# Optimization experiments

Measured on AMD Instinct MI355X. Metric: run time of the kernel, lower is better.

## Reference

```python
import jax, jax.numpy as jnp
import numpy as np

B, D, O, E, K, H = 8192, 1024, 1024, 8, 2, 512
LOAD_BALANCE_ALPHA = 0.01


def setup_inputs() -> dict:
    key = jax.random.key(0)
    ks = jax.random.split(key, 7)
    s = 0.02
    return {
        "x": jax.random.normal(ks[0], (B, D), dtype=jnp.float32),
        "gate_W": jax.random.normal(ks[1], (D, E), dtype=jnp.float32) * s,
        "gate_b": jnp.zeros((E,), dtype=jnp.float32),
        "W1": jax.random.normal(ks[2], (E, D, H), dtype=jnp.float32) * s,
        "b1": jnp.zeros((E, H), dtype=jnp.float32),
        "W2": jax.random.normal(ks[3], (E, H, O), dtype=jnp.float32) * s,
        "b2": jnp.zeros((E, O), dtype=jnp.float32),
    }


def reference(x, gate_W, gate_b, W1, b1, W2, b2):
    # Gating (eval mode: no gate noise)
    gate_logits = x @ gate_W + gate_b                      # [B, E]
    top_v, top_i = jax.lax.top_k(gate_logits, K)           # [B, K]
    top_gates = jax.nn.softmax(top_v, axis=-1)             # [B, K]

    # All-expert MLP (E is small; dense grouped GEMM instead of per-sample loop)
    h = jax.nn.relu(jnp.einsum('bd,edh->ebh', x, W1) + b1[:, None, :])   # [E, B, H]
    expert_out = jnp.einsum('ebh,eho->beo', h, W2) + b2[None, :, :]      # [B, E, O]

    # Gather top-k expert outputs and weighted-combine
    sel = jnp.take_along_axis(expert_out, top_i[:, :, None], axis=1)     # [B, K, O]
    output = jnp.einsum('bk,bko->bo', top_gates, sel)                    # [B, O]

    # Load-balance auxiliary loss
    gates = jax.nn.softmax(gate_logits, axis=-1)
    importance = gates.mean(axis=0)                        # [E]
    load_balance_loss = E * jnp.sum(importance ** 2)
    return output, LOAD_BALANCE_ALPHA * load_balance_loss
```

## Files before the change

kernel.cpp:

```cpp
#include <hip/hip_runtime.h>
#include <hip/hip_bf16.h>
#include <stdint.h>

#define BB 8192
#define DD 1024
#define EE 8
#define HH 512
#define OO 1024
#define NG 16

typedef __bf16 bf16_t;
typedef bf16_t bf16x8 __attribute__((ext_vector_type(8)));
typedef float f32x4 __attribute__((ext_vector_type(4)));
typedef uint32_t u32;

#define CSTRIDE 16

#define WS_CNT    1024
#define WS_PPREF  2048
#define WS_RIDX   4096
#define WS_RGATE  (4096 + NG*BB*4)
#define WS_XB     (2u<<20)
#define WS_W1T    (WS_XB + (size_t)BB*DD*2)
#define WS_W2T    (WS_W1T + (size_t)EE*HH*DD*2)
#define WS_H      (WS_W2T + (size_t)EE*OO*HH*2)

#define GL16(gsrc, ldst)                                                       \
  __builtin_amdgcn_global_load_lds(                                            \
      (const __attribute__((address_space(1))) void*)(gsrc),                   \
      (__attribute__((address_space(3))) void*)(ldst), 16, 0, 0)

__global__ __launch_bounds__(256) void k_prep(const float* __restrict__ W1,
                                              const float* __restrict__ W2,
                                              bf16_t* __restrict__ W1T,
                                              bf16_t* __restrict__ W2T) {
  __shared__ __align__(16) bf16_t t[64][72];
  int bid = blockIdx.x;
  const float* src; bf16_t* dst; int R, C; int tile;
  if (bid < 1024) {
    int e = bid >> 7; tile = bid & 127;
    src = W1 + (size_t)e * DD * HH; dst = W1T + (size_t)e * HH * DD;
    R = DD; C = HH;
  } else {
    bid -= 1024;
    int e = bid >> 7; tile = bid & 127;
    src = W2 + (size_t)e * HH * OO; dst = W2T + (size_t)e * OO * HH;
    R = HH; C = OO;
  }
  int tpc = C >> 6;
  int r0 = (tile / tpc) << 6, c0 = (tile % tpc) << 6;
  int tid = threadIdx.x;
  {
    int r = tid >> 2, cs = (tid & 3) << 4;
    const f32x4* sp = (const f32x4*)(src + (size_t)(r0 + r) * C + c0 + cs);
    #pragma unroll
    for (int q = 0; q < 4; ++q) {
      f32x4 v = sp[q];
      t[cs + q*4 + 0][r] = (bf16_t)v.x;
      t[cs + q*4 + 1][r] = (bf16_t)v.y;
      t[cs + q*4 + 2][r] = (bf16_t)v.z;
      t[cs + q*4 + 3][r] = (bf16_t)v.w;
    }
  }
  __syncthreads();
  {
    int c = tid >> 2, rs = (tid & 3) << 4;
    bf16_t* op = dst + (size_t)(c0 + c) * R + r0 + rs;
    const uint4* lp = (const uint4*)(&t[c][rs]);
    uint4 a0 = lp[0], a1 = lp[1];
    ((uint4*)op)[0] = a0;
    ((uint4*)op)[1] = a1;
  }
}

__global__ __launch_bounds__(1024, 8) void k_gate(const float* __restrict__ x,
                                                  const float* __restrict__ gW,
                                                  const float* __restrict__ gb,
                                                  float* __restrict__ imp,
                                                  u32* __restrict__ cnt,
                                                  int* __restrict__ ridx,
                                                  float* __restrict__ rgate,
                                                  bf16_t* __restrict__ xb) {
  __shared__ __align__(16) float gLds[EE * DD];
  __shared__ float s_imp[EE];
  __shared__ u32 s_hist[NG];
  __shared__ u32 s_base[NG];
  __shared__ int   s_lb[NG][32];
  __shared__ float s_lg[NG][32];
  int tid = threadIdx.x;
  if (tid < EE) s_imp[tid] = 0.f;
  if (tid < NG) s_hist[tid] = 0u;
  {
    const f32x4* gp = (const f32x4*)(gW + (size_t)tid * EE);
    f32x4 g0 = gp[0], g1 = gp[1];
    gLds[0 * DD + tid] = g0.x; gLds[1 * DD + tid] = g0.y;
    gLds[2 * DD + tid] = g0.z; gLds[3 * DD + tid] = g0.w;
    gLds[4 * DD + tid] = g1.x; gLds[5 * DD + tid] = g1.y;
    gLds[6 * DD + tid] = g1.z; gLds[7 * DD + tid] = g1.w;
  }
  __syncthreads();

  int lane = tid & 63, w = tid >> 6;
  int b = (blockIdx.x << 4) + w;
  const float* xrow = x + (size_t)b * DD;
  bf16_t* xbrow = xb + (size_t)b * DD;

  double acc[EE];
  #pragma unroll
  for (int e = 0; e < EE; ++e) acc[e] = 0.0;

  #pragma unroll
  for (int q = 0; q < 4; ++q) {
    int d0 = (q << 8) + (lane << 2);
    f32x4 xv = *(const f32x4*)(xrow + d0);
    bf16_t xc[4] = {(bf16_t)xv.x, (bf16_t)xv.y, (bf16_t)xv.z, (bf16_t)xv.w};
    *(uint2*)(xbrow + d0) = *(const uint2*)xc;
    #pragma unroll
    for (int e = 0; e < EE; ++e) {
      f32x4 gv = *(const f32x4*)(gLds + e * DD + d0);
      acc[e] += (double)xv.x * gv.x;
      acc[e] += (double)xv.y * gv.y;
      acc[e] += (double)xv.z * gv.z;
      acc[e] += (double)xv.w * gv.w;
    }
  }
  #pragma unroll
  for (int e = 0; e < EE; ++e) {
    #pragma unroll
    for (int off = 32; off > 0; off >>= 1) acc[e] += __shfl_xor(acc[e], off);
  }
  if (lane == 0) {
    float v[EE];
    float m = -1e30f;
    #pragma unroll
    for (int e = 0; e < EE; ++e) { v[e] = (float)acc[e] + gb[e]; m = fmaxf(m, v[e]); }
    float s = 0.f, p[EE];
    #pragma unroll
    for (int e = 0; e < EE; ++e) { p[e] = expf(v[e] - m); s += p[e]; }
    float inv = 1.f / s;
    #pragma unroll
    for (int e = 0; e < EE; ++e) atomicAdd(&s_imp[e], p[e] * inv);
    int i0 = 0; float b0 = v[0];
    #pragma unroll
    for (int e = 1; e < EE; ++e) if (v[e] > b0) { b0 = v[e]; i0 = e; }
    int i1 = -1; float b1v = -1e30f;
    #pragma unroll
    for (int e = 0; e < EE; ++e) if (e != i0 && v[e] > b1v) { b1v = v[e]; i1 = e; }
    float tt = expf(b1v - b0);
    float g0 = 1.f / (1.f + tt), g1 = tt / (1.f + tt);
    int ga = i0 * 2, gbq = i1 * 2 + 1;
    u32 p0 = atomicAdd(&s_hist[ga], 1u);
    s_lb[ga][p0] = b; s_lg[ga][p0] = g0;
    u32 p1 = atomicAdd(&s_hist[gbq], 1u);
    s_lb[gbq][p1] = b; s_lg[gbq][p1] = g1;
  }
  __syncthreads();
  if (tid < NG) s_base[tid] = atomicAdd(&cnt[tid * CSTRIDE], s_hist[tid]);
  if (tid < EE) atomicAdd(&imp[tid * CSTRIDE], s_imp[tid]);
  __syncthreads();
  if (tid < NG * 32) {
    int g = tid >> 5, k = tid & 31;
    if ((u32)k < s_hist[g]) {
      u32 pos = s_base[g] + (u32)k;
      ridx[g * BB + pos] = s_lb[g][k];
      rgate[g * BB + pos] = s_lg[g][k];
    }
  }
}

__global__ void k_loss(const float* __restrict__ imp, const u32* __restrict__ cnt,
                       u32* __restrict__ ppref, float* __restrict__ outloss) {
  int tid = threadIdx.x;
  float v = (tid < EE) ? imp[tid * CSTRIDE] * (1.f / BB) : 0.f;
  v = v * v;
  #pragma unroll
  for (int off = 32; off > 0; off >>= 1) v += __shfl_xor(v, off);
  if (tid == 0) {
    *outloss = 0.01f * (float)EE * v;
    u32 s = 0;
    for (int g = 0; g < NG; ++g) {
      ppref[g] = s;
      s += ((cnt[g * CSTRIDE] + 127u) >> 7) << 7;
    }
  }
}

__global__ __launch_bounds__(256, 4) void k_mlp1(const u32* __restrict__ cnt,
                                                 const u32* __restrict__ ppref,
                                                 const int* __restrict__ ridx,
                                                 const bf16_t* __restrict__ xb,
                                                 const bf16_t* __restrict__ W1T,
                                                 const float* __restrict__ b1,
                                                 bf16_t* __restrict__ Hc) {
  __shared__ __align__(16) bf16_t sA[128 * 64];
  __shared__ __align__(16) bf16_t sB[64 * 64];
  __shared__ int s_rb[128];

  int bid = blockIdx.x;
  int e = bid & 7;
  int widx = bid >> 3;
  int nt = widx & 7;
  int mt = (widx >> 3) & 63;
  int which = (widx >> 9) & 1;
  int g = e * 2 + which;
  int n = (int)cnt[g * CSTRIDE];
  int m0 = mt << 7;
  if (m0 >= n) return;
  int tid = threadIdx.x;
  if (tid < 128) {
    int i = m0 + tid;
    s_rb[tid] = ridx[g * BB + min(i, n - 1)];
  }
  __syncthreads();

  int lane = tid & 63, w = tid >> 6;
  int lrow = lane >> 3;
  int lcol = (((lane & 7) ^ lrow) << 3);
  int n0 = nt << 6;
  const bf16_t* w1b = W1T + (size_t)e * HH * DD + (size_t)n0 * DD;

  const bf16_t* aptr[4]; const bf16_t* bptr[2];
  #pragma unroll
  for (int q = 0; q < 4; ++q) {
    int r = w * 32 + q * 8 + lrow;
    aptr[q] = xb + (size_t)s_rb[r] * DD + lcol;
  }
  #pragma unroll
  for (int q = 0; q < 2; ++q) {
    int r = w * 16 + q * 8 + lrow;
    bptr[q] = w1b + (size_t)r * DD + lcol;
  }

  f32x4 acc[4][2];
  f32x4 zz = {0.f, 0.f, 0.f, 0.f};
  #pragma unroll
  for (int mm = 0; mm < 4; ++mm)
    #pragma unroll
    for (int nn = 0; nn < 2; ++nn) acc[mm][nn] = zz;

  int lr = lane & 15, lk = lane >> 4;
  int wr = w >> 1, wc = w & 1;
  int rsw = lr & 7;

  for (int kk = 0; kk < 16; ++kk) {
    #pragma unroll
    for (int q = 0; q < 4; ++q) {
      GL16(aptr[q], sA + (w * 32 + q * 8) * 64);
      aptr[q] += 64;
    }
    #pragma unroll
    for (int q = 0; q < 2; ++q) {
      GL16(bptr[q], sB + (w * 16 + q * 8) * 64);
      bptr[q] += 64;
    }
    __syncthreads();
    #pragma unroll
    for (int ks = 0; ks < 2; ++ks) {
      int swb = ((ks * 4 + lk) ^ rsw) << 3;
      bf16x8 af[4], bfr[2];
      #pragma unroll
      for (int mm = 0; mm < 4; ++mm)
        af[mm] = *(const bf16x8*)(sA + (wr * 64 + mm * 16 + lr) * 64 + swb);
      #pragma unroll
      for (int nn = 0; nn < 2; ++nn)
        bfr[nn] = *(const bf16x8*)(sB + (wc * 32 + nn * 16 + lr) * 64 + swb);
      #pragma unroll
      for (int mm = 0; mm < 4; ++mm)
        #pragma unroll
        for (int nn = 0; nn < 2; ++nn)
          acc[mm][nn] = __builtin_amdgcn_mfma_f32_16x16x32_bf16(bfr[nn], af[mm], acc[mm][nn], 0, 0, 0);
    }
    __syncthreads();
  }

  int hbase = (int)ppref[g] + m0;
  const float* b1p = b1 + (size_t)e * HH + n0;
  #pragma unroll
  for (int mm = 0; mm < 4; ++mm) {
    int m = wr * 64 + mm * 16 + lr;
    size_t hrow = (size_t)(hbase + m) * HH + n0;
    #pragma unroll
    for (int nn = 0; nn < 2; ++nn) {
      int h0l = wc * 32 + nn * 16 + lk * 4;
      bf16_t pk[4];
      #pragma unroll
      for (int j = 0; j < 4; ++j)
        pk[j] = (bf16_t)fmaxf(acc[mm][nn][j] + b1p[h0l + j], 0.f);
      *(uint2*)(Hc + hrow + h0l) = *(const uint2*)pk;
    }
  }
}

template <int ADD>
__global__ __launch_bounds__(256, 4) void k_mlp2(const u32* __restrict__ cnt,
                                                 const u32* __restrict__ ppref,
                                                 const int* __restrict__ ridx,
                                                 const float* __restrict__ rgate,
                                                 const bf16_t* __restrict__ Hc,
                                                 const bf16_t* __restrict__ W2T,
                                                 const float* __restrict__ b2,
                                                 float* __restrict__ out) {
  __shared__ __align__(16) bf16_t sA[128 * 64];
  __shared__ __align__(16) bf16_t sB[128 * 64];
  __shared__ int s_rb[128];
  __shared__ float s_rg[128];

  int bid = blockIdx.x;
  int e = bid & 7; int g = (e << 1) | ADD;
  int t2 = bid >> 3; int nt = t2 & 7; int mt = t2 >> 3;
  int n = (int)cnt[g * CSTRIDE];
  int m0 = mt << 7;
  if (m0 >= n) return;
  int tid = threadIdx.x;
  if (tid < 128) {
    int i = m0 + tid;
    int ic = min(i, n - 1);
    s_rb[tid] = ridx[g * BB + ic];
    s_rg[tid] = (i < n) ? rgate[g * BB + ic] : 0.f;
  }
  __syncthreads();

  int lane = tid & 63, w = tid >> 6;
  int lrow = lane >> 3;
  int lcol = (((lane & 7) ^ lrow) << 3);
  int n0 = nt << 7;
  int hbase = (int)ppref[g] + m0;
  const bf16_t* w2b = W2T + (size_t)e * OO * HH + (size_t)n0 * HH;

  const bf16_t* aptr[4]; const bf16_t* bptr[4];
  #pragma unroll
  for (int q = 0; q < 4; ++q) {
    int r = w * 32 + q * 8 + lrow;
    aptr[q] = Hc + (size_t)(hbase + r) * HH + lcol;
    bptr[q] = w2b + (size_t)r * HH + lcol;
  }

  f32x4 acc[4][4];
  f32x4 zz = {0.f, 0.f, 0.f, 0.f};
  #pragma unroll
  for (int mm = 0; mm < 4; ++mm)
    #pragma unroll
    for (int nn = 0; nn < 4; ++nn) acc[mm][nn] = zz;

  int lr = lane & 15, lk = lane >> 4;
  int wr = w >> 1, wc = w & 1;
  int rsw = lr & 7;

  for (int kk = 0; kk < 8; ++kk) {
    #pragma unroll
    for (int q = 0; q < 4; ++q) {
      GL16(aptr[q], sA + (w * 32 + q * 8) * 64);
      GL16(bptr[q], sB + (w * 32 + q * 8) * 64);
      aptr[q] += 64; bptr[q] += 64;
    }
    __syncthreads();
    #pragma unroll
    for (int ks = 0; ks < 2; ++ks) {
      int swb = ((ks * 4 + lk) ^ rsw) << 3;
      bf16x8 af[4], bfr[4];
      #pragma unroll
      for (int mm = 0; mm < 4; ++mm)
        af[mm] = *(const bf16x8*)(sA + (wr * 64 + mm * 16 + lr) * 64 + swb);
      #pragma unroll
      for (int nn = 0; nn < 4; ++nn)
        bfr[nn] = *(const bf16x8*)(sB + (wc * 64 + nn * 16 + lr) * 64 + swb);
      #pragma unroll
      for (int mm = 0; mm < 4; ++mm)
        #pragma unroll
        for (int nn = 0; nn < 4; ++nn)
          acc[mm][nn] = __builtin_amdgcn_mfma_f32_16x16x32_bf16(bfr[nn], af[mm], acc[mm][nn], 0, 0, 0);
    }
    __syncthreads();
  }

  const float* b2p = b2 + (size_t)e * OO + n0;
  #pragma unroll
  for (int mm = 0; mm < 4; ++mm) {
    int m = wr * 64 + mm * 16 + lr;
    if (m0 + m < n) {
      float gg = s_rg[m];
      float* orow = out + (size_t)s_rb[m] * OO + n0;
      #pragma unroll
      for (int nn = 0; nn < 4; ++nn) {
        int o0 = wc * 64 + nn * 16 + lk * 4;
        f32x4 v;
        #pragma unroll
        for (int j = 0; j < 4; ++j)
          v[j] = (acc[mm][nn][j] + b2p[o0 + j]) * gg;
        if (ADD) {
          f32x4 old = *(const f32x4*)(orow + o0);
          v += old;
        }
        *(f32x4*)(orow + o0) = v;
      }
    }
  }
}

extern "C" void kernel_launch(void* const* d_in, const int* in_sizes, int n_in,
                              void* d_out, int out_size, void* d_ws, size_t ws_size,
                              hipStream_t stream) {
  const float* x   = (const float*)d_in[0];
  const float* gW  = (const float*)d_in[1];
  const float* gb  = (const float*)d_in[2];
  const float* W1  = (const float*)d_in[3];
  const float* b1  = (const float*)d_in[4];
  const float* W2  = (const float*)d_in[5];
  const float* b2  = (const float*)d_in[6];
  float* out = (float*)d_out;

  uint8_t* ws = (uint8_t*)d_ws;
  float*   imp   = (float*)(ws + 0);
  u32*     cnt   = (u32*)(ws + WS_CNT);
  u32*     ppref = (u32*)(ws + WS_PPREF);
  int*     ridx  = (int*)(ws + WS_RIDX);
  float*   rgate = (float*)(ws + WS_RGATE);
  bf16_t*  xb    = (bf16_t*)(ws + WS_XB);
  bf16_t*  W1T   = (bf16_t*)(ws + WS_W1T);
  bf16_t*  W2T   = (bf16_t*)(ws + WS_W2T);
  bf16_t*  Hc    = (bf16_t*)(ws + WS_H);

  hipMemsetAsync(ws, 0, 4096, stream);

  k_prep<<<2048, 256, 0, stream>>>(W1, W2, W1T, W2T);
  k_gate<<<512, 1024, 0, stream>>>(x, gW, gb, imp, cnt, ridx, rgate, xb);
  k_loss<<<1, 64, 0, stream>>>(imp, cnt, ppref, out + (size_t)BB * OO);
  k_mlp1<<<8 * 2 * 64 * 8, 256, 0, stream>>>(cnt, ppref, ridx, xb, W1T, b1, Hc);
  k_mlp2<0><<<EE * 8 * 64, 256, 0, stream>>>(cnt, ppref, ridx, rgate, Hc, W2T, b2, out);
  k_mlp2<1><<<EE * 8 * 64, 256, 0, stream>>>(cnt, ppref, ridx, rgate, Hc, W2T, b2, out);
}
```

Baseline: 123.0 us.

## Fuse gating with weight prep, fold loss into mlp1, shrink mlp2 M-tile

The weight transpose/convert kernel and the gating kernel are merged into one launch, with gating blocks shrunk to 256 threads and a shared-memory union so both kinds of block can share the grid. The loss/prefix kernel is removed: block 0 of mlp1 computes the loss, and each GEMM block recomputes its padded row-group base from the counts. mlp2 moves to a 64-row M tile, doubling the grid, to reduce padded work and improve occupancy. This cuts launch overhead and lets prep overlap with gating, at the cost of a serial per-block prefix loop and more B-tile reloads in mlp2.

New measurement: 152.6 us. 1.24x slower.

```diff
diff --git a/kernel.cpp b/kernel.cpp
--- a/kernel.cpp
+++ b/kernel.cpp
@@ -17,7 +17,6 @@
 #define CSTRIDE 16
 
 #define WS_CNT    1024
-#define WS_PPREF  2048
 #define WS_RIDX   4096
 #define WS_RGATE  (4096 + NG*BB*4)
 #define WS_XB     (2u<<20)
@@ -30,173 +29,180 @@
       (const __attribute__((address_space(1))) void*)(gsrc),                   \
       (__attribute__((address_space(3))) void*)(ldst), 16, 0, 0)
 
-__global__ __launch_bounds__(256) void k_prep(const float* __restrict__ W1,
-                                              const float* __restrict__ W2,
-                                              bf16_t* __restrict__ W1T,
-                                              bf16_t* __restrict__ W2T) {
-  __shared__ __align__(16) bf16_t t[64][72];
-  int bid = blockIdx.x;
-  const float* src; bf16_t* dst; int R, C; int tile;
-  if (bid < 1024) {
-    int e = bid >> 7; tile = bid & 127;
-    src = W1 + (size_t)e * DD * HH; dst = W1T + (size_t)e * HH * DD;
-    R = DD; C = HH;
-  } else {
-    bid -= 1024;
-    int e = bid >> 7; tile = bid & 127;
-    src = W2 + (size_t)e * HH * OO; dst = W2T + (size_t)e * OO * HH;
-    R = HH; C = OO;
-  }
-  int tpc = C >> 6;
-  int r0 = (tile / tpc) << 6, c0 = (tile % tpc) << 6;
-  int tid = threadIdx.x;
-  {
-    int r = tid >> 2, cs = (tid & 3) << 4;
-    const f32x4* sp = (const f32x4*)(src + (size_t)(r0 + r) * C + c0 + cs);
-    #pragma unroll
-    for (int q = 0; q < 4; ++q) {
-      f32x4 v = sp[q];
-      t[cs + q*4 + 0][r] = (bf16_t)v.x;
-      t[cs + q*4 + 1][r] = (bf16_t)v.y;
-      t[cs + q*4 + 2][r] = (bf16_t)v.z;
-      t[cs + q*4 + 3][r] = (bf16_t)v.w;
-    }
-  }
-  __syncthreads();
-  {
-    int c = tid >> 2, rs = (tid & 3) << 4;
-    bf16_t* op = dst + (size_t)(c0 + c) * R + r0 + rs;
-    const uint4* lp = (const uint4*)(&t[c][rs]);
-    uint4 a0 = lp[0], a1 = lp[1];
-    ((uint4*)op)[0] = a0;
-    ((uint4*)op)[1] = a1;
-  }
-}
-
-__global__ __launch_bounds__(1024, 8) void k_gate(const float* __restrict__ x,
+union SmemU {
+  struct {
+    float gLds[EE * DD];
+    float s_imp[EE];
+    u32   s_hist[NG];
+    u32   s_base[NG];
+    int   s_lb[NG][8];
+    float s_lg[NG][8];
+  } g;
+  struct {
+    bf16_t t[64][72];
+  } p;
+};
+
+__global__ __launch_bounds__(256, 4) void k_fused(const float* __restrict__ x,
                                                   const float* __restrict__ gW,
                                                   const float* __restrict__ gb,
+                                                  const float* __restrict__ W1,
+                                                  const float* __restrict__ W2,
                                                   float* __restrict__ imp,
                                                   u32* __restrict__ cnt,
                                                   int* __restrict__ ridx,
                                                   float* __restrict__ rgate,
-                                                  bf16_t* __restrict__ xb) {
-  __shared__ __align__(16) float gLds[EE * DD];
-  __shared__ float s_imp[EE];
-  __shared__ u32 s_hist[NG];
-  __shared__ u32 s_base[NG];
-  __shared__ int   s_lb[NG][32];
-  __shared__ float s_lg[NG][32];
+                                                  bf16_t* __restrict__ xb,
+                                                  bf16_t* __restrict__ W1T,
+                                                  bf16_t* __restrict__ W2T) {
+  __shared__ SmemU sm;
   int tid = threadIdx.x;
-  if (tid < EE) s_imp[tid] = 0.f;
-  if (tid < NG) s_hist[tid] = 0u;
-  {
-    const f32x4* gp = (const f32x4*)(gW + (size_t)tid * EE);
-    f32x4 g0 = gp[0], g1 = gp[1];
-    gLds[0 * DD + tid] = g0.x; gLds[1 * DD + tid] = g0.y;
-    gLds[2 * DD + tid] = g0.z; gLds[3 * DD + tid] = g0.w;
-    gLds[4 * DD + tid] = g1.x; gLds[5 * DD + tid] = g1.y;
-    gLds[6 * DD + tid] = g1.z; gLds[7 * DD + tid] = g1.w;
-  }
-  __syncthreads();
-
-  int lane = tid & 63, w = tid >> 6;
-  int b = (blockIdx.x << 4) + w;
-  const float* xrow = x + (size_t)b * DD;
-  bf16_t* xbrow = xb + (size_t)b * DD;
-
-  double acc[EE];
-  #pragma unroll
-  for (int e = 0; e < EE; ++e) acc[e] = 0.0;
-
-  #pragma unroll
-  for (int q = 0; q < 4; ++q) {
-    int d0 = (q << 8) + (lane << 2);
-    f32x4 xv = *(const f32x4*)(xrow + d0);
-    bf16_t xc[4] = {(bf16_t)xv.x, (bf16_t)xv.y, (bf16_t)xv.z, (bf16_t)xv.w};
-    *(uint2*)(xbrow + d0) = *(const uint2*)xc;
+  int bid = blockIdx.x;
+
+  if (bid < 2048) {
+    if (tid < EE) sm.g.s_imp[tid] = 0.f;
+    if (tid < NG) sm.g.s_hist[tid] = 0u;
+    #pragma unroll
+    for (int i = 0; i < 4; ++i) {
+      int d = tid + (i << 8);
+      const f32x4* gp = (const f32x4*)(gW + (size_t)d * EE);
+      f32x4 g0 = gp[0], g1 = gp[1];
+      sm.g.gLds[0 * DD + d] = g0.x; sm.g.gLds[1 * DD + d] = g0.y;
+      sm.g.gLds[2 * DD + d] = g0.z; sm.g.gLds[3 * DD + d] = g0.w;
+      sm.g.gLds[4 * DD + d] = g1.x; sm.g.gLds[5 * DD + d] = g1.y;
+      sm.g.gLds[6 * DD + d] = g1.z; sm.g.gLds[7 * DD + d] = g1.w;
+    }
+    __syncthreads();
+
+    int lane = tid & 63, w = tid >> 6;
+    int b = (bid << 2) + w;
+    const float* xrow = x + (size_t)b * DD;
+    bf16_t* xbrow = xb + (size_t)b * DD;
+
+    double acc[EE];
+    #pragma unroll
+    for (int e = 0; e < EE; ++e) acc[e] = 0.0;
+
+    #pragma unroll
+    for (int q = 0; q < 4; ++q) {
+      int d0 = (q << 8) + (lane << 2);
+      f32x4 xv = *(const f32x4*)(xrow + d0);
+      bf16_t xc[4] = {(bf16_t)xv.x, (bf16_t)xv.y, (bf16_t)xv.z, (bf16_t)xv.w};
+      *(uint2*)(xbrow + d0) = *(const uint2*)xc;
+      #pragma unroll
+      for (int e = 0; e < EE; ++e) {
+        f32x4 gv = *(const f32x4*)(sm.g.gLds + e * DD + d0);
+        acc[e] += (double)xv.x * gv.x;
+        acc[e] += (double)xv.y * gv.y;
+        acc[e] += (double)xv.z * gv.z;
+        acc[e] += (double)xv.w * gv.w;
+      }
+    }
     #pragma unroll
     for (int e = 0; e < EE; ++e) {
-      f32x4 gv = *(const f32x4*)(gLds + e * DD + d0);
-      acc[e] += (double)xv.x * gv.x;
-      acc[e] += (double)xv.y * gv.y;
-      acc[e] += (double)xv.z * gv.z;
-      acc[e] += (double)xv.w * gv.w;
-    }
-  }
-  #pragma unroll
-  for (int e = 0; e < EE; ++e) {
-    #pragma unroll
-    for (int off = 32; off > 0; off >>= 1) acc[e] += __shfl_xor(acc[e], off);
-  }
-  if (lane == 0) {
-    float v[EE];
-    float m = -1e30f;
-    #pragma unroll
-    for (int e = 0; e < EE; ++e) { v[e] = (float)acc[e] + gb[e]; m = fmaxf(m, v[e]); }
-    float s = 0.f, p[EE];
-    #pragma unroll
-    for (int e = 0; e < EE; ++e) { p[e] = expf(v[e] - m); s += p[e]; }
-    float inv = 1.f / s;
-    #pragma unroll
-    for (int e = 0; e < EE; ++e) atomicAdd(&s_imp[e], p[e] * inv);
-    int i0 = 0; float b0 = v[0];
-    #pragma unroll
-    for (int e = 1; e < EE; ++e) if (v[e] > b0) { b0 = v[e]; i0 = e; }
-    int i1 = -1; float b1v = -1e30f;
-    #pragma unroll
-    for (int e = 0; e < EE; ++e) if (e != i0 && v[e] > b1v) { b1v = v[e]; i1 = e; }
-    float tt = expf(b1v - b0);
-    float g0 = 1.f / (1.f + tt), g1 = tt / (1.f + tt);
-    int ga = i0 * 2, gbq = i1 * 2 + 1;
-    u32 p0 = atomicAdd(&s_hist[ga], 1u);
-    s_lb[ga][p0] = b; s_lg[ga][p0] = g0;
-    u32 p1 = atomicAdd(&s_hist[gbq], 1u);
-    s_lb[gbq][p1] = b; s_lg[gbq][p1] = g1;
-  }
-  __syncthreads();
-  if (tid < NG) s_base[tid] = atomicAdd(&cnt[tid * CSTRIDE], s_hist[tid]);
-  if (tid < EE) atomicAdd(&imp[tid * CSTRIDE], s_imp[tid]);
-  __syncthreads();
-  if (tid < NG * 32) {
-    int g = tid >> 5, k = tid & 31;
-    if ((u32)k < s_hist[g]) {
-      u32 pos = s_base[g] + (u32)k;
-      ridx[g * BB + pos] = s_lb[g][k];
-      rgate[g * BB + pos] = s_lg[g][k];
+      #pragma unroll
+      for (int off = 32; off > 0; off >>= 1) acc[e] += __shfl_xor(acc[e], off);
+    }
+    if (lane == 0) {
+      float v[EE];
+      float m = -1e30f;
+      #pragma unroll
+      for (int e = 0; e < EE; ++e) { v[e] = (float)acc[e] + gb[e]; m = fmaxf(m, v[e]); }
+      float s = 0.f, p[EE];
+      #pragma unroll
+      for (int e = 0; e < EE; ++e) { p[e] = expf(v[e] - m); s += p[e]; }
+      float inv = 1.f / s;
+      #pragma unroll
+      for (int e = 0; e < EE; ++e) atomicAdd(&sm.g.s_imp[e], p[e] * inv);
+      int i0 = 0; float b0 = v[0];
+      #pragma unroll
+      for (int e = 1; e < EE; ++e) if (v[e] > b0) { b0 = v[e]; i0 = e; }
+      int i1 = -1; float b1v = -1e30f;
+      #pragma unroll
+      for (int e = 0; e < EE; ++e) if (e != i0 && v[e] > b1v) { b1v = v[e]; i1 = e; }
+      float tt = expf(b1v - b0);
+      float g0 = 1.f / (1.f + tt), g1 = tt / (1.f + tt);
+      int ga = i0 * 2, gbq = i1 * 2 + 1;
+      u32 p0 = atomicAdd(&sm.g.s_hist[ga], 1u);
+      sm.g.s_lb[ga][p0] = b; sm.g.s_lg[ga][p0] = g0;
+      u32 p1 = atomicAdd(&sm.g.s_hist[gbq], 1u);
+      sm.g.s_lb[gbq][p1] = b; sm.g.s_lg[gbq][p1] = g1;
+    }
+    __syncthreads();
+    if (tid < NG) sm.g.s_base[tid] = atomicAdd(&cnt[tid * CSTRIDE], sm.g.s_hist[tid]);
+    if (tid < EE) atomicAdd(&imp[tid * CSTRIDE], sm.g.s_imp[tid]);
+    __syncthreads();
+    if (tid < NG * 8) {
+      int g = tid >> 3, k = tid & 7;
+      if ((u32)k < sm.g.s_hist[g]) {
+        u32 pos = sm.g.s_base[g] + (u32)k;
+        ridx[g * BB + pos] = sm.g.s_lb[g][k];
+        rgate[g * BB + pos] = sm.g.s_lg[g][k];
+      }
+    }
+  } else {
+    int pbid = bid - 2048;
+    const float* src; bf16_t* dst; int R, C; int tile;
+    if (pbid < 1024) {
+      int e = pbid >> 7; tile = pbid & 127;
+      src = W1 + (size_t)e * DD * HH; dst = W1T + (size_t)e * HH * DD;
+      R = DD; C = HH;
+    } else {
+      pbid -= 1024;
+      int e = pbid >> 7; tile = pbid & 127;
+      src = W2 + (size_t)e * HH * OO; dst = W2T + (size_t)e * OO * HH;
+      R = HH; C = OO;
+    }
+    int tpc = C >> 6;
+    int r0 = (tile / tpc) << 6, c0 = (tile % tpc) << 6;
+    {
+      int r = tid >> 2, cs = (tid & 3) << 4;
+      const f32x4* sp = (const f32x4*)(src + (size_t)(r0 + r) * C + c0 + cs);
+      #pragma unroll
+      for (int q = 0; q < 4; ++q) {
+        f32x4 v = sp[q];
+        sm.p.t[cs + q*4 + 0][r] = (bf16_t)v.x;
+        sm.p.t[cs + q*4 + 1][r] = (bf16_t)v.y;
+        sm.p.t[cs + q*4 + 2][r] = (bf16_t)v.z;
+        sm.p.t[cs + q*4 + 3][r] = (bf16_t)v.w;
+      }
+    }
+    __syncthreads();
+    {
+      int c = tid >> 2, rs = (tid & 3) << 4;
+      bf16_t* op = dst + (size_t)(c0 + c) * R + r0 + rs;
+      const uint4* lp = (const uint4*)(&sm.p.t[c][rs]);
+      uint4 a0 = lp[0], a1 = lp[1];
+      ((uint4*)op)[0] = a0;
+      ((uint4*)op)[1] = a1;
     }
   }
 }
 
-__global__ void k_loss(const float* __restrict__ imp, const u32* __restrict__ cnt,
-                       u32* __restrict__ ppref, float* __restrict__ outloss) {
-  int tid = threadIdx.x;
-  float v = (tid < EE) ? imp[tid * CSTRIDE] * (1.f / BB) : 0.f;
-  v = v * v;
-  #pragma unroll
-  for (int off = 32; off > 0; off >>= 1) v += __shfl_xor(v, off);
-  if (tid == 0) {
-    *outloss = 0.01f * (float)EE * v;
-    u32 s = 0;
-    for (int g = 0; g < NG; ++g) {
-      ppref[g] = s;
-      s += ((cnt[g * CSTRIDE] + 127u) >> 7) << 7;
-    }
-  }
-}
-
 __global__ __launch_bounds__(256, 4) void k_mlp1(const u32* __restrict__ cnt,
-                                                 const u32* __restrict__ ppref,
+                                                 const float* __restrict__ imp,
                                                  const int* __restrict__ ridx,
                                                  const bf16_t* __restrict__ xb,
                                                  const bf16_t* __restrict__ W1T,
                                                  const float* __restrict__ b1,
-                                                 bf16_t* __restrict__ Hc) {
+                                                 bf16_t* __restrict__ Hc,
+                                                 float* __restrict__ out) {
   __shared__ __align__(16) bf16_t sA[128 * 64];
   __shared__ __align__(16) bf16_t sB[64 * 64];
   __shared__ int s_rb[128];
+  __shared__ int s_hb;
 
   int bid = blockIdx.x;
+  int tid = threadIdx.x;
+
+  if (bid == 0 && tid < 64) {
+    float v = (tid < EE) ? imp[tid * CSTRIDE] * (1.f / BB) : 0.f;
+    v = v * v;
+    #pragma unroll
+    for (int off = 32; off > 0; off >>= 1) v += __shfl_xor(v, off);
+    if (tid == 0) out[(size_t)BB * OO] = 0.01f * (float)EE * v;
+  }
+
   int e = bid & 7;
   int widx = bid >> 3;
   int nt = widx & 7;
@@ -206,7 +212,12 @@
   int n = (int)cnt[g * CSTRIDE];
   int m0 = mt << 7;
   if (m0 >= n) return;
-  int tid = threadIdx.x;
+  if (tid == 0) {
+    int hb = 0;
+    for (int g2 = 0; g2 < g; ++g2)
+      hb += (((int)cnt[g2 * CSTRIDE] + 127) >> 7) << 7;
+    s_hb = hb;
+  }
   if (tid < 128) {
     int i = m0 + tid;
     s_rb[tid] = ridx[g * BB + min(i, n - 1)];
@@ -273,7 +284,7 @@
     __syncthreads();
   }
 
-  int hbase = (int)ppref[g] + m0;
+  int hbase = s_hb + m0;
   const float* b1p = b1 + (size_t)e * HH + n0;
   #pragma unroll
   for (int mm = 0; mm < 4; ++mm) {
@@ -293,26 +304,32 @@
 
 template <int ADD>
 __global__ __launch_bounds__(256, 4) void k_mlp2(const u32* __restrict__ cnt,
-                                                 const u32* __restrict__ ppref,
                                                  const int* __restrict__ ridx,
                                                  const float* __restrict__ rgate,
                                                  const bf16_t* __restrict__ Hc,
                                                  const bf16_t* __restrict__ W2T,
                                                  const float* __restrict__ b2,
                                                  float* __restrict__ out) {
-  __shared__ __align__(16) bf16_t sA[128 * 64];
+  __shared__ __align__(16) bf16_t sA[64 * 64];
   __shared__ __align__(16) bf16_t sB[128 * 64];
-  __shared__ int s_rb[128];
-  __shared__ float s_rg[128];
+  __shared__ int s_rb[64];
+  __shared__ float s_rg[64];
+  __shared__ int s_hb;
 
   int bid = blockIdx.x;
   int e = bid & 7; int g = (e << 1) | ADD;
   int t2 = bid >> 3; int nt = t2 & 7; int mt = t2 >> 3;
   int n = (int)cnt[g * CSTRIDE];
-  int m0 = mt << 7;
+  int m0 = mt << 6;
   if (m0 >= n) return;
   int tid = threadIdx.x;
-  if (tid < 128) {
+  if (tid == 0) {
+    int hb = 0;
+    for (int g2 = 0; g2 < g; ++g2)
+      hb += (((int)cnt[g2 * CSTRIDE] + 127) >> 7) << 7;
+    s_hb = hb;
+  }
+  if (tid < 64) {
     int i = m0 + tid;
     int ic = min(i, n - 1);
     s_rb[tid] = ridx[g * BB + ic];
@@ -324,48 +341,56 @@
   int lrow = lane >> 3;
   int lcol = (((lane & 7) ^ lrow) << 3);
   int n0 = nt << 7;
-  int hbase = (int)ppref[g] + m0;
+  int hbase = s_hb + m0;
   const bf16_t* w2b = W2T + (size_t)e * OO * HH + (size_t)n0 * HH;
 
-  const bf16_t* aptr[4]; const bf16_t* bptr[4];
+  const bf16_t* aptr[2]; const bf16_t* bptr[4];
+  #pragma unroll
+  for (int q = 0; q < 2; ++q) {
+    int r = w * 16 + q * 8 + lrow;
+    aptr[q] = Hc + (size_t)(hbase + r) * HH + lcol;
+  }
   #pragma unroll
   for (int q = 0; q < 4; ++q) {
     int r = w * 32 + q * 8 + lrow;
-    aptr[q] = Hc + (size_t)(hbase + r) * HH + lcol;
     bptr[q] = w2b + (size_t)r * HH + lcol;
   }
 
-  f32x4 acc[4][4];
+  f32x4 acc[2][4];
   f32x4 zz = {0.f, 0.f, 0.f, 0.f};
   #pragma unroll
-  for (int mm = 0; mm < 4; ++mm)
+  for (int mm = 0; mm < 2; ++mm)
     #pragma unroll
     for (int nn = 0; nn < 4; ++nn) acc[mm][nn] = zz;
 
   int lr = lane & 15, lk = lane >> 4;
-  int wr = w >> 1, wc = w & 1;
+  int wr = w & 1, wc = w >> 1;
   int rsw = lr & 7;
 
   for (int kk = 0; kk < 8; ++kk) {
     #pragma unroll
+    for (int q = 0; q < 2; ++q) {
+      GL16(aptr[q], sA + (w * 16 + q * 8) * 64);
+      aptr[q] += 64;
+    }
+    #pragma unroll
     for (int q = 0; q < 4; ++q) {
-      GL16(aptr[q], sA + (w * 32 + q * 8) * 64);
       GL16(bptr[q], sB + (w * 32 + q * 8) * 64);
-      aptr[q] += 64; bptr[q] += 64;
+      bptr[q] += 64;
     }
     __syncthreads();
     #pragma unroll
     for (int ks = 0; ks < 2; ++ks) {
       int swb = ((ks * 4 + lk) ^ rsw) << 3;
-      bf16x8 af[4], bfr[4];
-      #pragma unroll
-      for (int mm = 0; mm < 4; ++mm)
-        af[mm] = *(const bf16x8*)(sA + (wr * 64 + mm * 16 + lr) * 64 + swb);
+      bf16x8 af[2], bfr[4];
+      #pragma unroll
+      for (int mm = 0; mm < 2; ++mm)
+        af[mm] = *(const bf16x8*)(sA + (wr * 32 + mm * 16 + lr) * 64 + swb);
       #pragma unroll
       for (int nn = 0; nn < 4; ++nn)
         bfr[nn] = *(const bf16x8*)(sB + (wc * 64 + nn * 16 + lr) * 64 + swb);
       #pragma unroll
-      for (int mm = 0; mm < 4; ++mm)
+      for (int mm = 0; mm < 2; ++mm)
         #pragma unroll
         for (int nn = 0; nn < 4; ++nn)
           acc[mm][nn] = __builtin_amdgcn_mfma_f32_16x16x32_bf16(bfr[nn], af[mm], acc[mm][nn], 0, 0, 0);
@@ -375,8 +400,8 @@
 
   const float* b2p = b2 + (size_t)e * OO + n0;
   #pragma unroll
-  for (int mm = 0; mm < 4; ++mm) {
-    int m = wr * 64 + mm * 16 + lr;
+  for (int mm = 0; mm < 2; ++mm) {
+    int m = wr * 32 + mm * 16 + lr;
     if (m0 + m < n) {
       float gg = s_rg[m];
       float* orow = out + (size_t)s_rb[m] * OO + n0;
@@ -412,7 +437,6 @@
   uint8_t* ws = (uint8_t*)d_ws;
   float*   imp   = (float*)(ws + 0);
   u32*     cnt   = (u32*)(ws + WS_CNT);
-  u32*     ppref = (u32*)(ws + WS_PPREF);
   int*     ridx  = (int*)(ws + WS_RIDX);
   float*   rgate = (float*)(ws + WS_RGATE);
   bf16_t*  xb    = (bf16_t*)(ws + WS_XB);
@@ -420,12 +444,11 @@
   bf16_t*  W2T   = (bf16_t*)(ws + WS_W2T);
   bf16_t*  Hc    = (bf16_t*)(ws + WS_H);
 
-  hipMemsetAsync(ws, 0, 4096, stream);
-
-  k_prep<<<2048, 256, 0, stream>>>(W1, W2, W1T, W2T);
-  k_gate<<<512, 1024, 0, stream>>>(x, gW, gb, imp, cnt, ridx, rgate, xb);
-  k_loss<<<1, 64, 0, stream>>>(imp, cnt, ppref, out + (size_t)BB * OO);
-  k_mlp1<<<8 * 2 * 64 * 8, 256, 0, stream>>>(cnt, ppref, ridx, xb, W1T, b1, Hc);
-  k_mlp2<0><<<EE * 8 * 64, 256, 0, stream>>>(cnt, ppref, ridx, rgate, Hc, W2T, b2, out);
-  k_mlp2<1><<<EE * 8 * 64, 256, 0, stream>>>(cnt, ppref, ridx, rgate, Hc, W2T, b2, out);
+  hipMemsetAsync(ws, 0, 2048, stream);
+
+  k_fused<<<4096, 256, 0, stream>>>(x, gW, gb, W1, W2, imp, cnt, ridx, rgate,
+                                    xb, W1T, W2T);
+  k_mlp1<<<8192, 256, 0, stream>>>(cnt, imp, ridx, xb, W1T, b1, Hc, out);
+  k_mlp2<0><<<8192, 256, 0, stream>>>(cnt, ridx, rgate, Hc, W2T, b2, out);
+  k_mlp2<1><<<8192, 256, 0, stream>>>(cnt, ridx, rgate, Hc, W2T, b2, out);
 }
```

## Fold loss kernel into mlp1 and shrink mlp2 M-tile to 64 rows

Applied to the files above, without the earlier changes.

Removes the separate single-block loss/prefix kernel: block 0 of k_mlp1 computes the load-balance loss, and each block of mlp1/mlp2 computes its padded group base from the counts directly. k_mlp2 switches from 128-row to 64-row M tiles with twice as many blocks, so partially filled expert groups waste less work and more blocks are available. The smaller tile lowers per-block reuse of W2 data and adds a short serial prefix loop in every block.

Result: no change. 124.5 us (+1.2%).

```diff
diff --git a/kernel.cpp b/kernel.cpp
--- a/kernel.cpp
+++ b/kernel.cpp
@@ -17,7 +17,6 @@
 #define CSTRIDE 16
 
 #define WS_CNT    1024
-#define WS_PPREF  2048
 #define WS_RIDX   4096
 #define WS_RGATE  (4096 + NG*BB*4)
 #define WS_XB     (2u<<20)
@@ -168,35 +167,30 @@
   }
 }
 
-__global__ void k_loss(const float* __restrict__ imp, const u32* __restrict__ cnt,
-                       u32* __restrict__ ppref, float* __restrict__ outloss) {
-  int tid = threadIdx.x;
-  float v = (tid < EE) ? imp[tid * CSTRIDE] * (1.f / BB) : 0.f;
-  v = v * v;
-  #pragma unroll
-  for (int off = 32; off > 0; off >>= 1) v += __shfl_xor(v, off);
-  if (tid == 0) {
-    *outloss = 0.01f * (float)EE * v;
-    u32 s = 0;
-    for (int g = 0; g < NG; ++g) {
-      ppref[g] = s;
-      s += ((cnt[g * CSTRIDE] + 127u) >> 7) << 7;
-    }
-  }
-}
-
 __global__ __launch_bounds__(256, 4) void k_mlp1(const u32* __restrict__ cnt,
-                                                 const u32* __restrict__ ppref,
+                                                 const float* __restrict__ imp,
                                                  const int* __restrict__ ridx,
                                                  const bf16_t* __restrict__ xb,
                                                  const bf16_t* __restrict__ W1T,
                                                  const float* __restrict__ b1,
-                                                 bf16_t* __restrict__ Hc) {
+                                                 bf16_t* __restrict__ Hc,
+                                                 float* __restrict__ out) {
   __shared__ __align__(16) bf16_t sA[128 * 64];
   __shared__ __align__(16) bf16_t sB[64 * 64];
   __shared__ int s_rb[128];
+  __shared__ int s_hb;
 
   int bid = blockIdx.x;
+  int tid = threadIdx.x;
+
+  if (bid == 0 && tid < 64) {
+    float v = (tid < EE) ? imp[tid * CSTRIDE] * (1.f / BB) : 0.f;
+    v = v * v;
+    #pragma unroll
+    for (int off = 32; off > 0; off >>= 1) v += __shfl_xor(v, off);
+    if (tid == 0) out[(size_t)BB * OO] = 0.01f * (float)EE * v;
+  }
+
   int e = bid & 7;
   int widx = bid >> 3;
   int nt = widx & 7;
@@ -206,7 +200,12 @@
   int n = (int)cnt[g * CSTRIDE];
   int m0 = mt << 7;
   if (m0 >= n) return;
-  int tid = threadIdx.x;
+  if (tid == 0) {
+    int hb = 0;
+    for (int g2 = 0; g2 < g; ++g2)
+      hb += (((int)cnt[g2 * CSTRIDE] + 127) >> 7) << 7;
+    s_hb = hb;
+  }
   if (tid < 128) {
     int i = m0 + tid;
     s_rb[tid] = ridx[g * BB + min(i, n - 1)];
@@ -273,7 +272,7 @@
     __syncthreads();
   }
 
-  int hbase = (int)ppref[g] + m0;
+  int hbase = s_hb + m0;
   const float* b1p = b1 + (size_t)e * HH + n0;
   #pragma unroll
   for (int mm = 0; mm < 4; ++mm) {
@@ -293,26 +292,32 @@
 
 template <int ADD>
 __global__ __launch_bounds__(256, 4) void k_mlp2(const u32* __restrict__ cnt,
-                                                 const u32* __restrict__ ppref,
                                                  const int* __restrict__ ridx,
                                                  const float* __restrict__ rgate,
                                                  const bf16_t* __restrict__ Hc,
                                                  const bf16_t* __restrict__ W2T,
                                                  const float* __restrict__ b2,
                                                  float* __restrict__ out) {
-  __shared__ __align__(16) bf16_t sA[128 * 64];
+  __shared__ __align__(16) bf16_t sA[64 * 64];
   __shared__ __align__(16) bf16_t sB[128 * 64];
-  __shared__ int s_rb[128];
-  __shared__ float s_rg[128];
+  __shared__ int s_rb[64];
+  __shared__ float s_rg[64];
+  __shared__ int s_hb;
 
   int bid = blockIdx.x;
   int e = bid & 7; int g = (e << 1) | ADD;
   int t2 = bid >> 3; int nt = t2 & 7; int mt = t2 >> 3;
   int n = (int)cnt[g * CSTRIDE];
-  int m0 = mt << 7;
+  int m0 = mt << 6;
   if (m0 >= n) return;
   int tid = threadIdx.x;
-  if (tid < 128) {
+  if (tid == 0) {
+    int hb = 0;
+    for (int g2 = 0; g2 < g; ++g2)
+      hb += (((int)cnt[g2 * CSTRIDE] + 127) >> 7) << 7;
+    s_hb = hb;
+  }
+  if (tid < 64) {
     int i = m0 + tid;
     int ic = min(i, n - 1);
     s_rb[tid] = ridx[g * BB + ic];
@@ -324,48 +329,56 @@
   int lrow = lane >> 3;
   int lcol = (((lane & 7) ^ lrow) << 3);
   int n0 = nt << 7;
-  int hbase = (int)ppref[g] + m0;
+  int hbase = s_hb + m0;
   const bf16_t* w2b = W2T + (size_t)e * OO * HH + (size_t)n0 * HH;
 
-  const bf16_t* aptr[4]; const bf16_t* bptr[4];
+  const bf16_t* aptr[2]; const bf16_t* bptr[4];
+  #pragma unroll
+  for (int q = 0; q < 2; ++q) {
+    int r = w * 16 + q * 8 + lrow;
+    aptr[q] = Hc + (size_t)(hbase + r) * HH + lcol;
+  }
   #pragma unroll
   for (int q = 0; q < 4; ++q) {
     int r = w * 32 + q * 8 + lrow;
-    aptr[q] = Hc + (size_t)(hbase + r) * HH + lcol;
     bptr[q] = w2b + (size_t)r * HH + lcol;
   }
 
-  f32x4 acc[4][4];
+  f32x4 acc[2][4];
   f32x4 zz = {0.f, 0.f, 0.f, 0.f};
   #pragma unroll
-  for (int mm = 0; mm < 4; ++mm)
+  for (int mm = 0; mm < 2; ++mm)
     #pragma unroll
     for (int nn = 0; nn < 4; ++nn) acc[mm][nn] = zz;
 
   int lr = lane & 15, lk = lane >> 4;
-  int wr = w >> 1, wc = w & 1;
+  int wr = w & 1, wc = w >> 1;
   int rsw = lr & 7;
 
   for (int kk = 0; kk < 8; ++kk) {
     #pragma unroll
+    for (int q = 0; q < 2; ++q) {
+      GL16(aptr[q], sA + (w * 16 + q * 8) * 64);
+      aptr[q] += 64;
+    }
+    #pragma unroll
     for (int q = 0; q < 4; ++q) {
-      GL16(aptr[q], sA + (w * 32 + q * 8) * 64);
       GL16(bptr[q], sB + (w * 32 + q * 8) * 64);
-      aptr[q] += 64; bptr[q] += 64;
+      bptr[q] += 64;
     }
     __syncthreads();
     #pragma unroll
     for (int ks = 0; ks < 2; ++ks) {
       int swb = ((ks * 4 + lk) ^ rsw) << 3;
-      bf16x8 af[4], bfr[4];
-      #pragma unroll
-      for (int mm = 0; mm < 4; ++mm)
-        af[mm] = *(const bf16x8*)(sA + (wr * 64 + mm * 16 + lr) * 64 + swb);
+      bf16x8 af[2], bfr[4];
+      #pragma unroll
+      for (int mm = 0; mm < 2; ++mm)
+        af[mm] = *(const bf16x8*)(sA + (wr * 32 + mm * 16 + lr) * 64 + swb);
       #pragma unroll
       for (int nn = 0; nn < 4; ++nn)
         bfr[nn] = *(const bf16x8*)(sB + (wc * 64 + nn * 16 + lr) * 64 + swb);
       #pragma unroll
-      for (int mm = 0; mm < 4; ++mm)
+      for (int mm = 0; mm < 2; ++mm)
         #pragma unroll
         for (int nn = 0; nn < 4; ++nn)
           acc[mm][nn] = __builtin_amdgcn_mfma_f32_16x16x32_bf16(bfr[nn], af[mm], acc[mm][nn], 0, 0, 0);
@@ -375,8 +388,8 @@
 
   const float* b2p = b2 + (size_t)e * OO + n0;
   #pragma unroll
-  for (int mm = 0; mm < 4; ++mm) {
-    int m = wr * 64 + mm * 16 + lr;
+  for (int mm = 0; mm < 2; ++mm) {
+    int m = wr * 32 + mm * 16 + lr;
     if (m0 + m < n) {
       float gg = s_rg[m];
       float* orow = out + (size_t)s_rb[m] * OO + n0;
@@ -412,7 +425,6 @@
   uint8_t* ws = (uint8_t*)d_ws;
   float*   imp   = (float*)(ws + 0);
   u32*     cnt   = (u32*)(ws + WS_CNT);
-  u32*     ppref = (u32*)(ws + WS_PPREF);
   int*     ridx  = (int*)(ws + WS_RIDX);
   float*   rgate = (float*)(ws + WS_RGATE);
   bf16_t*  xb    = (bf16_t*)(ws + WS_XB);
@@ -420,12 +432,11 @@
   bf16_t*  W2T   = (bf16_t*)(ws + WS_W2T);
   bf16_t*  Hc    = (bf16_t*)(ws + WS_H);
 
-  hipMemsetAsync(ws, 0, 4096, stream);
+  hipMemsetAsync(ws, 0, 2048, stream);
 
   k_prep<<<2048, 256, 0, stream>>>(W1, W2, W1T, W2T);
   k_gate<<<512, 1024, 0, stream>>>(x, gW, gb, imp, cnt, ridx, rgate, xb);
-  k_loss<<<1, 64, 0, stream>>>(imp, cnt, ppref, out + (size_t)BB * OO);
-  k_mlp1<<<8 * 2 * 64 * 8, 256, 0, stream>>>(cnt, ppref, ridx, xb, W1T, b1, Hc);
-  k_mlp2<0><<<EE * 8 * 64, 256, 0, stream>>>(cnt, ppref, ridx, rgate, Hc, W2T, b2, out);
-  k_mlp2<1><<<EE * 8 * 64, 256, 0, stream>>>(cnt, ppref, ridx, rgate, Hc, W2T, b2, out);
+  k_mlp1<<<8192, 256, 0, stream>>>(cnt, imp, ridx, xb, W1T, b1, Hc, out);
+  k_mlp2<0><<<8192, 256, 0, stream>>>(cnt, ridx, rgate, Hc, W2T, b2, out);
+  k_mlp2<1><<<8192, 256, 0, stream>>>(cnt, ridx, rgate, Hc, W2T, b2, out);
 }
```
